# Optimization experiments

Measured on AMD Instinct MI355X. Metric: run time of the kernel, lower is better.

Reference implementation:

```python
import jax, jax.numpy as jnp
import numpy as np

EPS = 1e-5

def _proj(x, w, b, gamma, beta, mean, var):
    # 1x1 conv (einsum over channels) + BatchNorm (inference) ; Dropout is identity in eval.
    y = jnp.einsum('bchw,oc->bohw', x, w) + b[None, :, None, None]
    scale = gamma * jax.lax.rsqrt(var + EPS)
    shift = beta - mean * scale
    return y * scale[None, :, None, None] + shift[None, :, None, None]

def _make_layer(key, cin, cout):
    k1, k2, k3, k4 = jax.random.split(key, 4)
    w = jax.random.normal(k1, (cout, cin), jnp.float32) * (1.0 / np.sqrt(cin))
    b = jax.random.normal(k2, (cout,), jnp.float32) * 0.01
    gamma = 1.0 + 0.1 * jax.random.normal(k3, (cout,), jnp.float32)
    beta = 0.1 * jax.random.normal(k4, (cout,), jnp.float32)
    mean = 0.05 * jax.random.normal(jax.random.fold_in(k1, 7), (cout,), jnp.float32)
    var = 0.5 + jax.random.uniform(jax.random.fold_in(k2, 7), (cout,), jnp.float32)
    return w, b, gamma, beta, mean, var

def setup_inputs() -> dict:
    key = jax.random.key(0)
    B, C, Ci, H, W = 4, 128, 64, 64, 64
    ks = jax.random.split(key, 6)
    inp = {
        'x1': jax.random.normal(ks[0], (B, C, H, W), jnp.float32),
        'x2': jax.random.normal(ks[1], (B, C, H, W), jnp.float32),
    }
    for name, k, cin, cout in [('theta', ks[2], C, Ci), ('phi', ks[3], C, Ci),
                               ('g', ks[4], C, Ci), ('wout', ks[5], Ci, C)]:
        w, b, gm, bt, mn, vr = _make_layer(k, cin, cout)
        inp.update({f'{name}_w': w, f'{name}_b': b, f'{name}_g': gm,
                    f'{name}_beta': bt, f'{name}_m': mn, f'{name}_v': vr})
    return inp

def reference(x1, x2,
              theta_w, theta_b, theta_g, theta_beta, theta_m, theta_v,
              phi_w, phi_b, phi_g, phi_beta, phi_m, phi_v,
              g_w, g_b, g_g, g_beta, g_m, g_v,
              wout_w, wout_b, wout_g, wout_beta, wout_m, wout_v):
    B, C, H, W = x1.shape
    N = H * W
    theta_x1 = _proj(x1, theta_w, theta_b, theta_g, theta_beta, theta_m, theta_v).reshape(B, -1, N)  # [B,Ci,N]
    phi_x2 = _proj(x2, phi_w, phi_b, phi_g, phi_beta, phi_m, phi_v).reshape(B, -1, N)                # [B,Ci,N]
    g_x2 = _proj(x2, g_w, g_b, g_g, g_beta, g_m, g_v).reshape(B, -1, N)                              # [B,Ci,N]
    # attention_map[b, n, m] = sum_c theta[b,c,n] * phi[b,c,m]
    attn = jax.nn.softmax(jnp.einsum('bcn,bcm->bnm', theta_x1, phi_x2), axis=-1)  # [B,N,N]
    out = jnp.einsum('bnm,bcm->bcn', attn, g_x2).reshape(B, -1, H, W)             # [B,Ci,H,W]
    out = _proj(out, wout_w, wout_b, wout_g, wout_beta, wout_m, wout_v)           # [B,C,H,W]
    return jnp.concatenate((out, x1), axis=1)                                     # [B,2C,H,W]
```

## Files before the change

kernel.cpp:

```cpp
#include <hip/hip_runtime.h>
#include <stdint.h>
#include <stddef.h>

#define EPS   1e-5f
#define CINCH 128
#define CI    64
#define NPIX  4096
#define KSPL  6
#define LOG2E 1.44269504088896340736f

typedef __bf16 bf16_t;
typedef _Float16 f16_t;
typedef bf16_t bf16x8 __attribute__((ext_vector_type(8)));
typedef f16_t  f16x8  __attribute__((ext_vector_type(8)));
typedef float  f32x4  __attribute__((ext_vector_type(4)));

typedef __attribute__((address_space(3))) unsigned int lds_u32;
typedef __attribute__((address_space(1))) const unsigned int glb_u32;

__device__ __forceinline__ f32x4 mfma16(bf16x8 a, bf16x8 b, f32x4 c) {
  return __builtin_amdgcn_mfma_f32_16x16x32_bf16(a, b, c, 0, 0, 0);
}
__device__ __forceinline__ f32x4 fzero4() {
  f32x4 z = {0.f, 0.f, 0.f, 0.f};
  return z;
}
__device__ __forceinline__ void gload16(const void* g, void* l) {
  __builtin_amdgcn_global_load_lds((glb_u32*)g, (lds_u32*)l, 16, 0, 0);
}


__global__ __launch_bounds__(256) void proj_theta(
    const float* __restrict__ x1,
    const float* __restrict__ w,  const float* __restrict__ bb,
    const float* __restrict__ gm, const float* __restrict__ bt,
    const float* __restrict__ mn, const float* __restrict__ vr,
    bf16_t* __restrict__ thetaT_h, bf16_t* __restrict__ thetaT_l,
    float* __restrict__ out)
{
  __shared__ float wT[CINCH][CI];
  __shared__ float bfold[CI];
  __shared__ float tileF[32][68];

  const int tid = threadIdx.x;
  const int b   = blockIdx.y;
  const int n0  = blockIdx.x * 32;

  for (int idx = tid; idx < CI * CINCH; idx += 256) {
    const int o = idx & 63, c = idx >> 6;
    const float sc = gm[o] * rsqrtf(vr[o] + EPS);
    wT[c][o] = w[o * CINCH + c] * sc * LOG2E;
    if (c == 0) bfold[o] = (bb[o] * sc + bt[o] - mn[o] * sc) * LOG2E;
  }
  __syncthreads();

  const int px = tid & 31;
  const int og = tid >> 5;
  const float* xb = x1 + (size_t)b * CINCH * NPIX + n0 + px;

  float acc[8];
#pragma unroll
  for (int j = 0; j < 8; ++j) acc[j] = 0.f;

#pragma unroll 4
  for (int c0 = 0; c0 < CINCH; c0 += 4) {
    float xv[4];
#pragma unroll
    for (int cc = 0; cc < 4; ++cc) xv[cc] = xb[(size_t)(c0 + cc) * NPIX];
#pragma unroll
    for (int cc = 0; cc < 4; ++cc) {
      const f32x4 w0 = *(const f32x4*)&wT[c0 + cc][og * 8];
      const f32x4 w1 = *(const f32x4*)&wT[c0 + cc][og * 8 + 4];
#pragma unroll
      for (int j = 0; j < 4; ++j) {
        acc[j]     += w0[j] * xv[cc];
        acc[j + 4] += w1[j] * xv[cc];
      }
    }
  }
#pragma unroll
  for (int j = 0; j < 8; ++j) tileF[px][og * 8 + j] = acc[j] + bfold[og * 8 + j];
  __syncthreads();

  {
    const int px2 = tid >> 3, ogs = tid & 7;
    bf16x8 hv, lv;
#pragma unroll
    for (int j = 0; j < 8; ++j) {
      const float v = tileF[px2][ogs * 8 + j];
      const bf16_t h = (bf16_t)v;
      hv[j] = h;
      lv[j] = (bf16_t)(v - (float)h);
    }
    const size_t base = ((size_t)b * NPIX + n0 + px2) * CI + ogs * 8;
    *(bf16x8*)(thetaT_h + base) = hv;
    *(bf16x8*)(thetaT_l + base) = lv;
  }

#pragma unroll
  for (int i = 0; i < 4; ++i) {
    const int idx = i * 256 + tid;
    const int c = idx >> 3, n4 = (idx & 7) * 4;
    *(f32x4*)(out + ((size_t)b * 256 + 128 + c) * NPIX + n0 + n4) =
        *(const f32x4*)(x1 + ((size_t)b * CINCH + c) * NPIX + n0 + n4);
  }
}

__global__ __launch_bounds__(256) void proj_phi(
    const float* __restrict__ x2,
    const float* __restrict__ w,  const float* __restrict__ bb,
    const float* __restrict__ gm, const float* __restrict__ bt,
    const float* __restrict__ mn, const float* __restrict__ vr,
    bf16_t* __restrict__ phiT_h, bf16_t* __restrict__ phiT_l)
{
  __shared__ float wT[CINCH][CI];
  __shared__ float bfold[CI];
  __shared__ float tileF[32][68];

  const int tid = threadIdx.x;
  const int b   = blockIdx.y;
  const int n0  = blockIdx.x * 32;

  for (int idx = tid; idx < CI * CINCH; idx += 256) {
    const int o = idx & 63, c = idx >> 6;
    const float sc = gm[o] * rsqrtf(vr[o] + EPS);
    wT[c][o] = w[o * CINCH + c] * sc;
    if (c == 0) bfold[o] = bb[o] * sc + bt[o] - mn[o] * sc;
  }
  __syncthreads();

  const int px = tid & 31;
  const int og = tid >> 5;
  const float* xb = x2 + (size_t)b * CINCH * NPIX + n0 + px;

  float acc[8];
#pragma unroll
  for (int j = 0; j < 8; ++j) acc[j] = 0.f;

#pragma unroll 4
  for (int c0 = 0; c0 < CINCH; c0 += 4) {
    float xv[4];
#pragma unroll
    for (int cc = 0; cc < 4; ++cc) xv[cc] = xb[(size_t)(c0 + cc) * NPIX];
#pragma unroll
    for (int cc = 0; cc < 4; ++cc) {
      const f32x4 w0 = *(const f32x4*)&wT[c0 + cc][og * 8];
      const f32x4 w1 = *(const f32x4*)&wT[c0 + cc][og * 8 + 4];
#pragma unroll
      for (int j = 0; j < 4; ++j) {
        acc[j]     += w0[j] * xv[cc];
        acc[j + 4] += w1[j] * xv[cc];
      }
    }
  }
#pragma unroll
  for (int j = 0; j < 8; ++j) tileF[px][og * 8 + j] = acc[j] + bfold[og * 8 + j];
  __syncthreads();

  {
    const int px2 = tid >> 3, ogs = tid & 7;
    const int n = n0 + px2;
    bf16x8 hv, lv;
#pragma unroll
    for (int j = 0; j < 8; ++j) {
      const float v = tileF[px2][ogs * 8 + j];
      const bf16_t h = (bf16_t)v;
      hv[j] = h;
      lv[j] = (bf16_t)(v - (float)h);
    }
    const size_t rowb = ((size_t)b * NPIX + n) * 128;
    const int byte = (ogs * 16) ^ ((n & 7) << 4);
    *(bf16x8*)((char*)phiT_h + rowb + byte) = hv;
    *(bf16x8*)((char*)phiT_l + rowb + byte) = lv;
  }
}

__global__ __launch_bounds__(256) void proj_g(
    const float* __restrict__ x2,
    const float* __restrict__ w,  const float* __restrict__ bb,
    const float* __restrict__ gm, const float* __restrict__ bt,
    const float* __restrict__ mn, const float* __restrict__ vr,
    bf16_t* __restrict__ g_cm)
{
  __shared__ float wT[CINCH][CI];
  __shared__ float bfold[CI];
  __shared__ float gT[CI][33];

  const int tid = threadIdx.x;
  const int b   = blockIdx.y;
  const int n0  = blockIdx.x * 32;

  for (int idx = tid; idx < CI * CINCH; idx += 256) {
    const int o = idx & 63, c = idx >> 6;
    const float sc = gm[o] * rsqrtf(vr[o] + EPS);
    wT[c][o] = w[o * CINCH + c] * sc;
    if (c == 0) bfold[o] = bb[o] * sc + bt[o] - mn[o] * sc;
  }
  __syncthreads();

  const int px = tid & 31;
  const int og = tid >> 5;
  const float* xb = x2 + (size_t)b * CINCH * NPIX + n0 + px;

  float acc[8];
#pragma unroll
  for (int j = 0; j < 8; ++j) acc[j] = 0.f;

#pragma unroll 4
  for (int c0 = 0; c0 < CINCH; c0 += 4) {
    float xv[4];
#pragma unroll
    for (int cc = 0; cc < 4; ++cc) xv[cc] = xb[(size_t)(c0 + cc) * NPIX];
#pragma unroll
    for (int cc = 0; cc < 4; ++cc) {
      const f32x4 w0 = *(const f32x4*)&wT[c0 + cc][og * 8];
      const f32x4 w1 = *(const f32x4*)&wT[c0 + cc][og * 8 + 4];
#pragma unroll
      for (int j = 0; j < 4; ++j) {
        acc[j]     += w0[j] * xv[cc];
        acc[j + 4] += w1[j] * xv[cc];
      }
    }
  }
#pragma unroll
  for (int j = 0; j < 8; ++j) gT[og * 8 + j][px] = acc[j] + bfold[og * 8 + j];
  __syncthreads();

  {
    const int c = tid & 63, mgp = tid >> 6;
    bf16x8 gv;
#pragma unroll
    for (int j = 0; j < 8; ++j) gv[j] = (bf16_t)gT[c][mgp * 8 + j];
    *(bf16x8*)(g_cm + ((size_t)b * CI + c) * NPIX + n0 + mgp * 8) = gv;
  }
}

__global__ __launch_bounds__(256, 3) void flash_attn(
    const bf16_t* __restrict__ thetaT_h, const bf16_t* __restrict__ thetaT_l,
    const bf16_t* __restrict__ phiT_h,   const bf16_t* __restrict__ phiT_l,
    const bf16_t* __restrict__ g_cm,
    f16_t* __restrict__ Opart, float* __restrict__ mlbuf)
{
  __shared__ __attribute__((aligned(16))) char sK[2][8192];
  __shared__ __attribute__((aligned(16))) char sV[2][64 * 80];
  __shared__ __attribute__((aligned(16))) char sP[4][32 * 80];

  const int tid  = threadIdx.x;
  const int lane = tid & 63;
  const int wid  = tid >> 6;
  const int lrow = lane & 15;
  const int lhi  = lane >> 4;

  const int wg = blockIdx.x;
  const int b  = wg / 192;
  const int rr = wg % 192;
  const int qt = rr / KSPL;
  const int ks = rr % KSPL;
  const int q0 = qt * 128 + wid * 32;
  const int t0 = (ks * 128) / KSPL;
  const int t1 = ((ks + 1) * 128) / KSPL;

  const char* const srcPHb = (const char*)phiT_h + ((size_t)b * NPIX) * 128;
  const char* const srcPLb = (const char*)phiT_l + ((size_t)b * NPIX) * 128;
  const char* const srcVb  = (const char*)g_cm + (size_t)b * CI * NPIX * 2;

  const int vc = tid >> 2, vp = tid & 3;

  auto stageK = [&](int buf, int tile) {
    const size_t rb = (size_t)tile * 32 * 128;
    gload16(srcPHb + rb + tid * 16, sK[buf] + tid * 16);
    gload16(srcPLb + rb + tid * 16, sK[buf] + 4096 + tid * 16);
  };
  auto loadV = [&](int tile) {
    return *(const f32x4*)(srcVb + ((size_t)vc * NPIX + tile * 32 + vp * 8) * 2);
  };
  auto writeV = [&](int buf, f32x4 v) {
    *(f32x4*)(sV[buf] + vc * 80 + vp * 16) = v;
  };

  bf16x8 qh[2][2], qlv[2][2];
  {
    const bf16_t* qbh = thetaT_h + ((size_t)b * NPIX + q0 + lrow) * CI + lhi * 8;
    const bf16_t* qbl = thetaT_l + ((size_t)b * NPIX + q0 + lrow) * CI + lhi * 8;
#pragma unroll
    for (int nt = 0; nt < 2; ++nt)
#pragma unroll
      for (int kk = 0; kk < 2; ++kk) {
        qh[nt][kk]  = *(const bf16x8*)(qbh + nt * 16 * CI + kk * 32);
        qlv[nt][kk] = *(const bf16x8*)(qbl + nt * 16 * CI + kk * 32);
      }
  }

  f32x4 oacc[2][4];
#pragma unroll
  for (int a = 0; a < 2; ++a)
#pragma unroll
    for (int c = 0; c < 4; ++c) oacc[a][c] = fzero4();

  float m_run[2] = {-1e30f, -1e30f};
  float l_run[2] = {0.f, 0.f};

  char* const Pw = sP[wid];

  stageK(0, t0);
  writeV(0, loadV(t0));
  __syncthreads();

  for (int t = t0; t < t1; ++t) {
    const int cur = (t - t0) & 1;
    const bool more = (t + 1 < t1);
    f32x4 vnext;
    if (more) { stageK(cur ^ 1, t + 1); vnext = loadV(t + 1); }

    const char* const sKH = sK[cur];
    const char* const sKL = sK[cur] + 4096;

    f32x4 s[2][2];
#pragma unroll
    for (int mt = 0; mt < 2; ++mt)
#pragma unroll
      for (int nt = 0; nt < 2; ++nt) s[mt][nt] = fzero4();

    __builtin_amdgcn_s_setprio(1);
#pragma unroll
    for (int mt = 0; mt < 2; ++mt) {
      const int row = mt * 16 + lrow;
      const int swz = (row & 7) << 4;
#pragma unroll
      for (int kk = 0; kk < 2; ++kk) {
        const int byte = row * 128 + ((kk * 64 + lhi * 16) ^ swz);
        const bf16x8 aH = *(const bf16x8*)(sKH + byte);
        const bf16x8 aL = *(const bf16x8*)(sKL + byte);
#pragma unroll
        for (int nt = 0; nt < 2; ++nt) {
          s[mt][nt] = mfma16(aH, qh[nt][kk],  s[mt][nt]);
          s[mt][nt] = mfma16(aH, qlv[nt][kk], s[mt][nt]);
          s[mt][nt] = mfma16(aL, qh[nt][kk],  s[mt][nt]);
        }
      }
    }
    __builtin_amdgcn_s_setprio(0);

    float a2[2];
#pragma unroll
    for (int nt = 0; nt < 2; ++nt) {
      float mx = fmaxf(fmaxf(fmaxf(s[0][nt][0], s[0][nt][1]),
                             fmaxf(s[0][nt][2], s[0][nt][3])),
                       fmaxf(fmaxf(s[1][nt][0], s[1][nt][1]),
                             fmaxf(s[1][nt][2], s[1][nt][3])));
      mx = fmaxf(mx, __shfl_xor(mx, 16));
      mx = fmaxf(mx, __shfl_xor(mx, 32));
      const float mnew  = fmaxf(m_run[nt], mx);
      const float alpha = exp2f(m_run[nt] - mnew);
      float lsum = 0.f;
#pragma unroll
      for (int mt = 0; mt < 2; ++mt)
#pragma unroll
        for (int r = 0; r < 4; ++r) {
          const float p = exp2f(s[mt][nt][r] - mnew);
          s[mt][nt][r] = p;
          lsum += p;
        }
      lsum += __shfl_xor(lsum, 16);
      lsum += __shfl_xor(lsum, 32);
      l_run[nt] = l_run[nt] * alpha + lsum;
      m_run[nt] = mnew;
      a2[nt] = alpha;
    }

#pragma unroll
    for (int qt2 = 0; qt2 < 2; ++qt2) {
#pragma unroll
      for (int r = 0; r < 4; ++r) {
        const float av = __shfl(a2[qt2], lhi * 4 + r);
#pragma unroll
        for (int ct = 0; ct < 4; ++ct) oacc[qt2][ct][r] *= av;
      }
    }

#pragma unroll
    for (int mt = 0; mt < 2; ++mt)
#pragma unroll
      for (int nt = 0; nt < 2; ++nt) {
        union { bf16_t h[4]; uint32_t u[2]; } pk;
#pragma unroll
        for (int r = 0; r < 4; ++r) pk.h[r] = (bf16_t)s[mt][nt][r];
        const int q    = nt * 16 + lrow;
        const int mloc = mt * 16 + lhi * 4;
        *(uint2*)(Pw + q * 80 + mloc * 2) = make_uint2(pk.u[0], pk.u[1]);
      }

    if (more) writeV(cur ^ 1, vnext);

    const char* const sVc = sV[cur];
    bf16x8 bV[4];
#pragma unroll
    for (int ct = 0; ct < 4; ++ct)
      bV[ct] = *(const bf16x8*)(sVc + (ct * 16 + lrow) * 80 + lhi * 16);

    __builtin_amdgcn_s_setprio(1);
#pragma unroll
    for (int qt2 = 0; qt2 < 2; ++qt2) {
      const bf16x8 pfrag = *(const bf16x8*)(Pw + (qt2 * 16 + lrow) * 80 + lhi * 16);
#pragma unroll
      for (int ct = 0; ct < 4; ++ct)
        oacc[qt2][ct] = mfma16(pfrag, bV[ct], oacc[qt2][ct]);
    }
    __builtin_amdgcn_s_setprio(0);

    if (more) __syncthreads();
  }

  f16_t* const Ob = Opart + ((size_t)(b * KSPL + ks) * NPIX) * 64;
#pragma unroll
  for (int qt2 = 0; qt2 < 2; ++qt2)
#pragma unroll
    for (int ct = 0; ct < 4; ++ct)
#pragma unroll
      for (int r = 0; r < 4; ++r) {
        const int q = q0 + qt2 * 16 + lhi * 4 + r;
        const int c = ct * 16 + lrow;
        Ob[(size_t)q * 64 + c] = (f16_t)oacc[qt2][ct][r];
      }
  if (lhi < 2) {
    const int q = q0 + lhi * 16 + lrow;
    const size_t base = ((size_t)(b * KSPL + ks) * NPIX + q) * 2;
    mlbuf[base]     = m_run[lhi];
    mlbuf[base + 1] = l_run[lhi];
  }
}

__global__ __launch_bounds__(256) void merge_out(
    const f16_t* __restrict__ Opart, const float* __restrict__ mlbuf,
    const float* __restrict__ ww,  const float* __restrict__ wb,
    const float* __restrict__ wg,  const float* __restrict__ wbt,
    const float* __restrict__ wm,  const float* __restrict__ wvv,
    float* __restrict__ out)
{
  __shared__ float wlds[128][64];
  __shared__ float bfw[128];
  __shared__ float mrg[32][68];

  const int tid = threadIdx.x;
  const int b   = blockIdx.y;
  const int n0  = blockIdx.x * 32;

  for (int idx = tid; idx < 128 * 64; idx += 256) {
    const int o = idx >> 6, c = idx & 63;
    const float sc = wg[o] * rsqrtf(wvv[o] + EPS);
    wlds[o][c] = ww[o * 64 + c] * sc;
    if (c == 0) bfw[o] = wb[o] * sc + wbt[o] - wm[o] * sc;
  }

  {
    const int px = tid & 31;
    const int cg = tid >> 5;
    const int q  = n0 + px;
    float mk[KSPL], lk[KSPL];
#pragma unroll
    for (int ks = 0; ks < KSPL; ++ks) {
      const size_t base = ((size_t)(b * KSPL + ks) * NPIX + q) * 2;
      mk[ks] = mlbuf[base];
      lk[ks] = mlbuf[base + 1];
    }
    float M = mk[0];
#pragma unroll
    for (int ks = 1; ks < KSPL; ++ks) M = fmaxf(M, mk[ks]);
    float al[KSPL]; float den = 0.f;
#pragma unroll
    for (int ks = 0; ks < KSPL; ++ks) { al[ks] = exp2f(mk[ks] - M); den += al[ks] * lk[ks]; }
    const float inv = 1.f / den;
#pragma unroll
    for (int ks = 0; ks < KSPL; ++ks) al[ks] *= inv;

    float r[8];
#pragma unroll
    for (int j = 0; j < 8; ++j) r[j] = 0.f;
#pragma unroll
    for (int ks = 0; ks < KSPL; ++ks) {
      const f16x8 p = *(const f16x8*)(Opart +
          ((size_t)(b * KSPL + ks) * NPIX + q) * 64 + cg * 8);
#pragma unroll
      for (int j = 0; j < 8; ++j) r[j] += (float)p[j] * al[ks];
    }
#pragma unroll
    for (int j = 0; j < 8; ++j) mrg[px][cg * 8 + j] = r[j];
  }
  __syncthreads();

  const int px = tid & 31;
  const int oh = tid >> 5;
  float acc[16];
#pragma unroll
  for (int j = 0; j < 16; ++j) acc[j] = 0.f;

#pragma unroll 4
  for (int c0 = 0; c0 < 64; c0 += 4) {
    const f32x4 m4 = *(const f32x4*)&mrg[px][c0];
#pragma unroll
    for (int j = 0; j < 16; ++j) {
      const f32x4 w4 = *(const f32x4*)&wlds[oh * 16 + j][c0];
      acc[j] += w4[0] * m4[0] + w4[1] * m4[1] + w4[2] * m4[2] + w4[3] * m4[3];
    }
  }
#pragma unroll
  for (int j = 0; j < 16; ++j) {
    const int o = oh * 16 + j;
    out[((size_t)b * 256 + o) * NPIX + n0 + px] = acc[j] + bfw[o];
  }
}

extern "C" void kernel_launch(void* const* d_in, const int* in_sizes, int n_in,
                              void* d_out, int out_size, void* d_ws, size_t ws_size,
                              hipStream_t stream) {
  (void)in_sizes; (void)n_in; (void)out_size; (void)ws_size;
  const float* x1  = (const float*)d_in[0];
  const float* x2  = (const float*)d_in[1];
  const float* tw  = (const float*)d_in[2];
  const float* tb  = (const float*)d_in[3];
  const float* tg  = (const float*)d_in[4];
  const float* tbt = (const float*)d_in[5];
  const float* tm  = (const float*)d_in[6];
  const float* tv  = (const float*)d_in[7];
  const float* pw  = (const float*)d_in[8];
  const float* pb  = (const float*)d_in[9];
  const float* pg  = (const float*)d_in[10];
  const float* pbt = (const float*)d_in[11];
  const float* pm  = (const float*)d_in[12];
  const float* pv  = (const float*)d_in[13];
  const float* gw  = (const float*)d_in[14];
  const float* gb  = (const float*)d_in[15];
  const float* gg  = (const float*)d_in[16];
  const float* gbt = (const float*)d_in[17];
  const float* gmn = (const float*)d_in[18];
  const float* gv  = (const float*)d_in[19];
  const float* ww  = (const float*)d_in[20];
  const float* wb  = (const float*)d_in[21];
  const float* wg  = (const float*)d_in[22];
  const float* wbt = (const float*)d_in[23];
  const float* wm  = (const float*)d_in[24];
  const float* wv  = (const float*)d_in[25];

  float* out = (float*)d_out;
  char*  ws  = (char*)d_ws;
  bf16_t* thetaT_h = (bf16_t*)(ws);
  bf16_t* thetaT_l = (bf16_t*)(ws + (size_t)(2)  * 1048576);
  bf16_t* phiT_h   = (bf16_t*)(ws + (size_t)(4)  * 1048576);
  bf16_t* phiT_l   = (bf16_t*)(ws + (size_t)(6)  * 1048576);
  bf16_t* g_cm     = (bf16_t*)(ws + (size_t)(8)  * 1048576);
  f16_t*  Opart    = (f16_t*) (ws + (size_t)(10) * 1048576);
  float*  mlbuf    = (float*) (ws + (size_t)(23) * 1048576);

  dim3 gp(128, 4);
  proj_theta<<<gp, 256, 0, stream>>>(x1, tw, tb, tg, tbt, tm, tv,
                                     thetaT_h, thetaT_l, out);
  proj_phi<<<gp, 256, 0, stream>>>(x2, pw, pb, pg, pbt, pm, pv,
                                   phiT_h, phiT_l);
  proj_g<<<gp, 256, 0, stream>>>(x2, gw, gb, gg, gbt, gmn, gv, g_cm);
  flash_attn<<<768, 256, 0, stream>>>(thetaT_h, thetaT_l, phiT_h, phiT_l,
                                      g_cm, Opart, mlbuf);
  merge_out<<<gp, 256, 0, stream>>>(Opart, mlbuf, ww, wb, wg, wbt, wm, wv, out);
}
```

Measured before the change: 238.3 us.

## Enlarge flash-attention tiles, skip unneeded rescales, stage projection inputs in LDS

The flash attention kernel now runs 512-thread workgroups covering 256 queries, with 64-key tiles, a KV split of 8, and XOR-swizzled LDS layouts for V and P in place of padded rows. The online softmax rescale of the output accumulators is skipped when no row maximum grew within the wave. The three projection kernels first load the input tile into LDS with coalesced vector loads, reusing that buffer for the output transpose, and theta copies x1 into the output during that load. The larger tiles and blocks raise LDS and register pressure per block and change the partial-output buffer layout, so the workspace offset for the softmax statistics moves.

After: 249.8 us. 1.05x slower.

```diff
diff --git a/kernel.cpp b/kernel.cpp
--- a/kernel.cpp
+++ b/kernel.cpp
@@ -6,7 +6,7 @@
 #define CINCH 128
 #define CI    64
 #define NPIX  4096
-#define KSPL  6
+#define KSPL  8
 #define LOG2E 1.44269504088896340736f
 
 typedef __bf16 bf16_t;
@@ -40,7 +40,9 @@
 {
   __shared__ float wT[CINCH][CI];
   __shared__ float bfold[CI];
-  __shared__ float tileF[32][68];
+  __shared__ __align__(16) char ubuf[CINCH * 32 * 4];
+  float (*xs)[32]    = (float(*)[32])ubuf;
+  float (*tileF)[68] = (float(*)[68])ubuf;
 
   const int tid = threadIdx.x;
   const int b   = blockIdx.y;
@@ -52,12 +54,23 @@
     wT[c][o] = w[o * CINCH + c] * sc * LOG2E;
     if (c == 0) bfold[o] = (bb[o] * sc + bt[o] - mn[o] * sc) * LOG2E;
   }
+
+  {
+    const float* xsrc = x1 + (size_t)b * CINCH * NPIX + n0;
+    float* osrc = out + ((size_t)b * 256 + 128) * NPIX + n0;
+#pragma unroll
+    for (int i = 0; i < 4; ++i) {
+      const int idx = i * 256 + tid;
+      const int c = idx >> 3, p = idx & 7;
+      const f32x4 v = *(const f32x4*)(xsrc + (size_t)c * NPIX + p * 4);
+      *(f32x4*)&xs[c][p * 4] = v;
+      *(f32x4*)(osrc + (size_t)c * NPIX + p * 4) = v;
+    }
+  }
   __syncthreads();
 
   const int px = tid & 31;
   const int og = tid >> 5;
-  const float* xb = x1 + (size_t)b * CINCH * NPIX + n0 + px;
-
   float acc[8];
 #pragma unroll
   for (int j = 0; j < 8; ++j) acc[j] = 0.f;
@@ -66,7 +79,7 @@
   for (int c0 = 0; c0 < CINCH; c0 += 4) {
     float xv[4];
 #pragma unroll
-    for (int cc = 0; cc < 4; ++cc) xv[cc] = xb[(size_t)(c0 + cc) * NPIX];
+    for (int cc = 0; cc < 4; ++cc) xv[cc] = xs[c0 + cc][px];
 #pragma unroll
     for (int cc = 0; cc < 4; ++cc) {
       const f32x4 w0 = *(const f32x4*)&wT[c0 + cc][og * 8];
@@ -78,6 +91,7 @@
       }
     }
   }
+  __syncthreads();
 #pragma unroll
   for (int j = 0; j < 8; ++j) tileF[px][og * 8 + j] = acc[j] + bfold[og * 8 + j];
   __syncthreads();
@@ -95,14 +109,6 @@
     const size_t base = ((size_t)b * NPIX + n0 + px2) * CI + ogs * 8;
     *(bf16x8*)(thetaT_h + base) = hv;
     *(bf16x8*)(thetaT_l + base) = lv;
-  }
-
-#pragma unroll
-  for (int i = 0; i < 4; ++i) {
-    const int idx = i * 256 + tid;
-    const int c = idx >> 3, n4 = (idx & 7) * 4;
-    *(f32x4*)(out + ((size_t)b * 256 + 128 + c) * NPIX + n0 + n4) =
-        *(const f32x4*)(x1 + ((size_t)b * CINCH + c) * NPIX + n0 + n4);
   }
 }
 
@@ -115,7 +121,9 @@
 {
   __shared__ float wT[CINCH][CI];
   __shared__ float bfold[CI];
-  __shared__ float tileF[32][68];
+  __shared__ __align__(16) char ubuf[CINCH * 32 * 4];
+  float (*xs)[32]    = (float(*)[32])ubuf;
+  float (*tileF)[68] = (float(*)[68])ubuf;
 
   const int tid = threadIdx.x;
   const int b   = blockIdx.y;
@@ -127,12 +135,19 @@
     wT[c][o] = w[o * CINCH + c] * sc;
     if (c == 0) bfold[o] = bb[o] * sc + bt[o] - mn[o] * sc;
   }
+  {
+    const float* xsrc = x2 + (size_t)b * CINCH * NPIX + n0;
+#pragma unroll
+    for (int i = 0; i < 4; ++i) {
+      const int idx = i * 256 + tid;
+      const int c = idx >> 3, p = idx & 7;
+      *(f32x4*)&xs[c][p * 4] = *(const f32x4*)(xsrc + (size_t)c * NPIX + p * 4);
+    }
+  }
   __syncthreads();
 
   const int px = tid & 31;
   const int og = tid >> 5;
-  const float* xb = x2 + (size_t)b * CINCH * NPIX + n0 + px;
-
   float acc[8];
 #pragma unroll
   for (int j = 0; j < 8; ++j) acc[j] = 0.f;
@@ -141,7 +156,7 @@
   for (int c0 = 0; c0 < CINCH; c0 += 4) {
     float xv[4];
 #pragma unroll
-    for (int cc = 0; cc < 4; ++cc) xv[cc] = xb[(size_t)(c0 + cc) * NPIX];
+    for (int cc = 0; cc < 4; ++cc) xv[cc] = xs[c0 + cc][px];
 #pragma unroll
     for (int cc = 0; cc < 4; ++cc) {
       const f32x4 w0 = *(const f32x4*)&wT[c0 + cc][og * 8];
@@ -153,6 +168,7 @@
       }
     }
   }
+  __syncthreads();
 #pragma unroll
   for (int j = 0; j < 8; ++j) tileF[px][og * 8 + j] = acc[j] + bfold[og * 8 + j];
   __syncthreads();
@@ -184,7 +200,9 @@
 {
   __shared__ float wT[CINCH][CI];
   __shared__ float bfold[CI];
-  __shared__ float gT[CI][33];
+  __shared__ __align__(16) char ubuf[CINCH * 32 * 4];
+  float (*xs)[32] = (float(*)[32])ubuf;
+  float (*gT)[33] = (float(*)[33])ubuf;
 
   const int tid = threadIdx.x;
   const int b   = blockIdx.y;
@@ -196,12 +214,19 @@
     wT[c][o] = w[o * CINCH + c] * sc;
     if (c == 0) bfold[o] = bb[o] * sc + bt[o] - mn[o] * sc;
   }
+  {
+    const float* xsrc = x2 + (size_t)b * CINCH * NPIX + n0;
+#pragma unroll
+    for (int i = 0; i < 4; ++i) {
+      const int idx = i * 256 + tid;
+      const int c = idx >> 3, p = idx & 7;
+      *(f32x4*)&xs[c][p * 4] = *(const f32x4*)(xsrc + (size_t)c * NPIX + p * 4);
+    }
+  }
   __syncthreads();
 
   const int px = tid & 31;
   const int og = tid >> 5;
-  const float* xb = x2 + (size_t)b * CINCH * NPIX + n0 + px;
-
   float acc[8];
 #pragma unroll
   for (int j = 0; j < 8; ++j) acc[j] = 0.f;
@@ -210,7 +235,7 @@
   for (int c0 = 0; c0 < CINCH; c0 += 4) {
     float xv[4];
 #pragma unroll
-    for (int cc = 0; cc < 4; ++cc) xv[cc] = xb[(size_t)(c0 + cc) * NPIX];
+    for (int cc = 0; cc < 4; ++cc) xv[cc] = xs[c0 + cc][px];
 #pragma unroll
     for (int cc = 0; cc < 4; ++cc) {
       const f32x4 w0 = *(const f32x4*)&wT[c0 + cc][og * 8];
@@ -222,6 +247,7 @@
       }
     }
   }
+  __syncthreads();
 #pragma unroll
   for (int j = 0; j < 8; ++j) gT[og * 8 + j][px] = acc[j] + bfold[og * 8 + j];
   __syncthreads();
@@ -235,15 +261,15 @@
   }
 }
 
-__global__ __launch_bounds__(256, 3) void flash_attn(
+__global__ __launch_bounds__(512, 4) void flash_attn(
     const bf16_t* __restrict__ thetaT_h, const bf16_t* __restrict__ thetaT_l,
     const bf16_t* __restrict__ phiT_h,   const bf16_t* __restrict__ phiT_l,
     const bf16_t* __restrict__ g_cm,
     f16_t* __restrict__ Opart, float* __restrict__ mlbuf)
 {
-  __shared__ __attribute__((aligned(16))) char sK[2][8192];
-  __shared__ __attribute__((aligned(16))) char sV[2][64 * 80];
-  __shared__ __attribute__((aligned(16))) char sP[4][32 * 80];
+  __shared__ __attribute__((aligned(16))) char sK[2][16384];
+  __shared__ __attribute__((aligned(16))) char sV[2][8192];
+  __shared__ __attribute__((aligned(16))) char sP[8][4096];
 
   const int tid  = threadIdx.x;
   const int lane = tid & 63;
@@ -252,30 +278,29 @@
   const int lhi  = lane >> 4;
 
   const int wg = blockIdx.x;
-  const int b  = wg / 192;
-  const int rr = wg % 192;
-  const int qt = rr / KSPL;
-  const int ks = rr % KSPL;
-  const int q0 = qt * 128 + wid * 32;
-  const int t0 = (ks * 128) / KSPL;
-  const int t1 = ((ks + 1) * 128) / KSPL;
+  const int b  = wg >> 7;
+  const int rr = wg & 127;
+  const int qt = rr >> 3;
+  const int ks = rr & 7;
+  const int q0 = qt * 256 + wid * 32;
+  const int tg0 = ks * 8;
 
   const char* const srcPHb = (const char*)phiT_h + ((size_t)b * NPIX) * 128;
   const char* const srcPLb = (const char*)phiT_l + ((size_t)b * NPIX) * 128;
   const char* const srcVb  = (const char*)g_cm + (size_t)b * CI * NPIX * 2;
 
-  const int vc = tid >> 2, vp = tid & 3;
-
-  auto stageK = [&](int buf, int tile) {
-    const size_t rb = (size_t)tile * 32 * 128;
+  const int vc = tid >> 3, vp = tid & 7;
+
+  auto stageK = [&](int buf, int tg) {
+    const size_t rb = (size_t)tg * 8192;
     gload16(srcPHb + rb + tid * 16, sK[buf] + tid * 16);
-    gload16(srcPLb + rb + tid * 16, sK[buf] + 4096 + tid * 16);
+    gload16(srcPLb + rb + tid * 16, sK[buf] + 8192 + tid * 16);
   };
-  auto loadV = [&](int tile) {
-    return *(const f32x4*)(srcVb + ((size_t)vc * NPIX + tile * 32 + vp * 8) * 2);
+  auto loadV = [&](int tg) {
+    return *(const f32x4*)(srcVb + ((size_t)vc * NPIX + tg * 64 + vp * 8) * 2);
   };
   auto writeV = [&](int buf, f32x4 v) {
-    *(f32x4*)(sV[buf] + vc * 80 + vp * 16) = v;
+    *(f32x4*)(sV[buf] + vc * 128 + ((vp * 16) ^ ((vc & 7) << 4))) = v;
   };
 
   bf16x8 qh[2][2], qlv[2][2];
@@ -301,29 +326,30 @@
   float l_run[2] = {0.f, 0.f};
 
   char* const Pw = sP[wid];
-
-  stageK(0, t0);
-  writeV(0, loadV(t0));
-  __syncthreads();
-
-  for (int t = t0; t < t1; ++t) {
-    const int cur = (t - t0) & 1;
-    const bool more = (t + 1 < t1);
+  const int pswz[2] = {(lrow & 7) << 4, ((lrow & 7) << 4)};
+
+  stageK(0, tg0);
+  writeV(0, loadV(tg0));
+  __syncthreads();
+
+  for (int t = 0; t < 8; ++t) {
+    const int cur = t & 1;
+    const bool more = (t < 7);
     f32x4 vnext;
-    if (more) { stageK(cur ^ 1, t + 1); vnext = loadV(t + 1); }
+    if (more) { stageK(cur ^ 1, tg0 + t + 1); vnext = loadV(tg0 + t + 1); }
 
     const char* const sKH = sK[cur];
-    const char* const sKL = sK[cur] + 4096;
-
-    f32x4 s[2][2];
-#pragma unroll
-    for (int mt = 0; mt < 2; ++mt)
+    const char* const sKL = sK[cur] + 8192;
+
+    f32x4 s[4][2];
+#pragma unroll
+    for (int mt = 0; mt < 4; ++mt)
 #pragma unroll
       for (int nt = 0; nt < 2; ++nt) s[mt][nt] = fzero4();
 
     __builtin_amdgcn_s_setprio(1);
 #pragma unroll
-    for (int mt = 0; mt < 2; ++mt) {
+    for (int mt = 0; mt < 4; ++mt) {
       const int row = mt * 16 + lrow;
       const int swz = (row & 7) << 4;
 #pragma unroll
@@ -341,20 +367,26 @@
     }
     __builtin_amdgcn_s_setprio(0);
 
-    float a2[2];
+    float mx[2], a2[2];
 #pragma unroll
     for (int nt = 0; nt < 2; ++nt) {
-      float mx = fmaxf(fmaxf(fmaxf(s[0][nt][0], s[0][nt][1]),
-                             fmaxf(s[0][nt][2], s[0][nt][3])),
-                       fmaxf(fmaxf(s[1][nt][0], s[1][nt][1]),
-                             fmaxf(s[1][nt][2], s[1][nt][3])));
-      mx = fmaxf(mx, __shfl_xor(mx, 16));
-      mx = fmaxf(mx, __shfl_xor(mx, 32));
-      const float mnew  = fmaxf(m_run[nt], mx);
-      const float alpha = exp2f(m_run[nt] - mnew);
+      float m1 = fmaxf(fmaxf(s[0][nt][0], s[0][nt][1]), fmaxf(s[0][nt][2], s[0][nt][3]));
+      float m2 = fmaxf(fmaxf(s[1][nt][0], s[1][nt][1]), fmaxf(s[1][nt][2], s[1][nt][3]));
+      float m3 = fmaxf(fmaxf(s[2][nt][0], s[2][nt][1]), fmaxf(s[2][nt][2], s[2][nt][3]));
+      float m4 = fmaxf(fmaxf(s[3][nt][0], s[3][nt][1]), fmaxf(s[3][nt][2], s[3][nt][3]));
+      float m = fmaxf(fmaxf(m1, m2), fmaxf(m3, m4));
+      m = fmaxf(m, __shfl_xor(m, 16));
+      m = fmaxf(m, __shfl_xor(m, 32));
+      mx[nt] = m;
+    }
+    const bool up = !__all((mx[0] <= m_run[0]) && (mx[1] <= m_run[1]));
+#pragma unroll
+    for (int nt = 0; nt < 2; ++nt) {
+      const float mnew  = up ? fmaxf(m_run[nt], mx[nt]) : m_run[nt];
+      const float alpha = up ? exp2f(m_run[nt] - mnew) : 1.f;
       float lsum = 0.f;
 #pragma unroll
-      for (int mt = 0; mt < 2; ++mt)
+      for (int mt = 0; mt < 4; ++mt)
 #pragma unroll
         for (int r = 0; r < 4; ++r) {
           const float p = exp2f(s[mt][nt][r] - mnew);
@@ -368,18 +400,20 @@
       a2[nt] = alpha;
     }
 
-#pragma unroll
-    for (int qt2 = 0; qt2 < 2; ++qt2) {
-#pragma unroll
-      for (int r = 0; r < 4; ++r) {
-        const float av = __shfl(a2[qt2], lhi * 4 + r);
-#pragma unroll
-        for (int ct = 0; ct < 4; ++ct) oacc[qt2][ct][r] *= av;
-      }
-    }
-
-#pragma unroll
-    for (int mt = 0; mt < 2; ++mt)
+    if (up) {
+#pragma unroll
+      for (int qt2 = 0; qt2 < 2; ++qt2) {
+#pragma unroll
+        for (int r = 0; r < 4; ++r) {
+          const float av = __shfl(a2[qt2], lhi * 4 + r);
+#pragma unroll
+          for (int ct = 0; ct < 4; ++ct) oacc[qt2][ct][r] *= av;
+        }
+      }
+    }
+
+#pragma unroll
+    for (int mt = 0; mt < 4; ++mt)
 #pragma unroll
       for (int nt = 0; nt < 2; ++nt) {
         union { bf16_t h[4]; uint32_t u[2]; } pk;
@@ -387,24 +421,34 @@
         for (int r = 0; r < 4; ++r) pk.h[r] = (bf16_t)s[mt][nt][r];
         const int q    = nt * 16 + lrow;
         const int mloc = mt * 16 + lhi * 4;
-        *(uint2*)(Pw + q * 80 + mloc * 2) = make_uint2(pk.u[0], pk.u[1]);
+        const int byte = q * 128 + ((mloc * 2) ^ ((q & 7) << 4));
+        *(uint2*)(Pw + byte) = make_uint2(pk.u[0], pk.u[1]);
       }
 
     if (more) writeV(cur ^ 1, vnext);
 
     const char* const sVc = sV[cur];
-    bf16x8 bV[4];
-#pragma unroll
-    for (int ct = 0; ct < 4; ++ct)
-      bV[ct] = *(const bf16x8*)(sVc + (ct * 16 + lrow) * 80 + lhi * 16);
-
+    bf16x8 bV[2][4];
+#pragma unroll
+    for (int ct = 0; ct < 4; ++ct) {
+      const int row = ct * 16 + lrow;
+      const int swz = (row & 7) << 4;
+#pragma unroll
+      for (int kk = 0; kk < 2; ++kk)
+        bV[kk][ct] = *(const bf16x8*)(sVc + row * 128 + ((kk * 64 + lhi * 16) ^ swz));
+    }
     __builtin_amdgcn_s_setprio(1);
 #pragma unroll
     for (int qt2 = 0; qt2 < 2; ++qt2) {
-      const bf16x8 pfrag = *(const bf16x8*)(Pw + (qt2 * 16 + lrow) * 80 + lhi * 16);
-#pragma unroll
-      for (int ct = 0; ct < 4; ++ct)
-        oacc[qt2][ct] = mfma16(pfrag, bV[ct], oacc[qt2][ct]);
+      const int q = qt2 * 16 + lrow;
+#pragma unroll
+      for (int kk = 0; kk < 2; ++kk) {
+        const bf16x8 pfrag =
+            *(const bf16x8*)(Pw + q * 128 + ((kk * 64 + lhi * 16) ^ ((q & 7) << 4)));
+#pragma unroll
+        for (int ct = 0; ct < 4; ++ct)
+          oacc[qt2][ct] = mfma16(pfrag, bV[kk][ct], oacc[qt2][ct]);
+      }
     }
     __builtin_amdgcn_s_setprio(0);
 
@@ -549,7 +593,7 @@
   bf16_t* phiT_l   = (bf16_t*)(ws + (size_t)(6)  * 1048576);
   bf16_t* g_cm     = (bf16_t*)(ws + (size_t)(8)  * 1048576);
   f16_t*  Opart    = (f16_t*) (ws + (size_t)(10) * 1048576);
-  float*  mlbuf    = (float*) (ws + (size_t)(23) * 1048576);
+  float*  mlbuf    = (float*) (ws + (size_t)(26) * 1048576);
 
   dim3 gp(128, 4);
   proj_theta<<<gp, 256, 0, stream>>>(x1, tw, tb, tg, tbt, tm, tv,
@@ -557,7 +601,7 @@
   proj_phi<<<gp, 256, 0, stream>>>(x2, pw, pb, pg, pbt, pm, pv,
                                    phiT_h, phiT_l);
   proj_g<<<gp, 256, 0, stream>>>(x2, gw, gb, gg, gbt, gmn, gv, g_cm);
-  flash_attn<<<768, 256, 0, stream>>>(thetaT_h, thetaT_l, phiT_h, phiT_l,
+  flash_attn<<<512, 512, 0, stream>>>(thetaT_h, thetaT_l, phiT_h, phiT_l,
                                       g_cm, Opart, mlbuf);
   merge_out<<<gp, 256, 0, stream>>>(Opart, mlbuf, ww, wb, wg, wbt, wm, wv, out);
 }
```
